# Kernel tuning notes

Measured on AMD Instinct MI355X. Metric: run time of the kernel, lower is better.

The kernel has to match this reference:

```python
import jax, jax.numpy as jnp
import numpy as np

N_NODES = 200000
N_EDGES = 12800000
C = 5  # channels
RADIUS = 0.05
CONSUME_RADIUS = RADIUS * 2
ACCEL_SCALE = 0.01
MAX_VEL = 0.1
CONSUME_EDGES_REQ = 3
EDGES_TO_STAY_ALIVE = 1
NEG_SLOPE = 0.2  # GATConv leaky_relu slope


def setup_inputs() -> dict:
    key = jax.random.key(0)
    ks = jax.random.split(key, 16)
    x = jax.random.normal(ks[0], (N_NODES, C), dtype=jnp.float32) * 0.1
    # column 4 is node type: 1 = cell, 0 = food
    is_cell = jax.random.bernoulli(ks[1], 0.9, (N_NODES,)).astype(jnp.float32)
    x = x.at[:, 4].set(is_cell)
    edge_index = jax.random.randint(ks[2], (2, N_EDGES), 0, N_NODES, dtype=jnp.int32)
    # edge_attr: [distance, is_cell_edge]
    dist = jax.random.uniform(ks[3], (N_EDGES,), dtype=jnp.float32) * 0.2
    cell_edge = jax.random.bernoulli(ks[4], 0.8, (N_EDGES,)).astype(jnp.float32)
    edge_attr = jnp.stack([dist, cell_edge], axis=1)
    s = 1.0 / np.sqrt(C)
    W = jax.random.normal(ks[5], (C, C), dtype=jnp.float32) * s        # GAT lin (shared src/dst)
    att_src = jax.random.normal(ks[6], (C,), dtype=jnp.float32) * s
    att_dst = jax.random.normal(ks[7], (C,), dtype=jnp.float32) * s
    We = jax.random.normal(ks[8], (2, C), dtype=jnp.float32) * 0.7      # lin_edge
    att_edge = jax.random.normal(ks[9], (C,), dtype=jnp.float32) * s
    gat_bias = jnp.zeros((C,), dtype=jnp.float32)
    W1 = jax.random.normal(ks[10], (C, C), dtype=jnp.float32) * s
    b1 = jnp.zeros((C,), dtype=jnp.float32)
    W2 = jax.random.normal(ks[11], (C, 2), dtype=jnp.float32) * s
    b2 = jnp.zeros((2,), dtype=jnp.float32)
    return {"x": x, "edge_index": edge_index, "edge_attr": edge_attr,
            "W": W, "att_src": att_src, "att_dst": att_dst, "We": We,
            "att_edge": att_edge, "gat_bias": gat_bias,
            "W1": W1, "b1": b1, "W2": W2, "b2": b2}


def _gat_conv(x, edge_index, edge_attr, W, att_src, att_dst, We, att_edge, gat_bias):
    # PyG GATConv, heads=1, edge_dim=2: softmax over incoming edges of each dst node
    n = x.shape[0]
    src, dst = edge_index[0], edge_index[1]
    hs = x @ W                                   # [N, C]
    a_src = hs @ att_src                         # [N]
    a_dst = hs @ att_dst                         # [N]
    a_e = (edge_attr @ We) @ att_edge            # [E]
    logits = jax.nn.leaky_relu(a_src[src] + a_dst[dst] + a_e, NEG_SLOPE)  # [E]
    m = jax.ops.segment_max(logits, dst, num_segments=n)                  # [N]
    ev = jnp.exp(logits - m[dst])
    denom = jax.ops.segment_sum(ev, dst, num_segments=n)                  # [N]
    alpha = ev / jnp.maximum(denom, 1e-16)[dst]
    out = jax.ops.segment_sum(hs[src] * alpha[:, None], dst, num_segments=n)
    return out + gat_bias


def reference(x, edge_index, edge_attr, W, att_src, att_dst, We, att_edge, gat_bias, W1, b1, W2, b2):
    n = x.shape[0]
    src = edge_index[0]
    # convolve: GAT -> MLP -> *2-1
    h = _gat_conv(x, edge_index, edge_attr, W, att_src, att_dst, We, att_edge, gat_bias)
    h = jax.nn.relu(jax.nn.relu(h @ W1 + b1) @ W2 + b2)
    h = h * 2.0 - 1.0                             # [N, 2]
    # only cells (type==1) accelerate
    food_mask = (x[:, 4] == 1).astype(jnp.float32)
    accel = h * ACCEL_SCALE * food_mask[:, None]
    velocity = jnp.clip(x[:, 2:4] + accel, -MAX_VEL, MAX_VEL)
    positions = x[:, :2] + velocity
    new_x = jnp.concatenate([positions, velocity, x[:, 4:]], axis=1)  # [N, 5]
    # border cost
    eps = 1e-6
    out_mask = (jnp.abs(positions) > 1).astype(jnp.float32)
    border_cost = jnp.sum(jnp.log(jnp.abs(positions) + eps) * out_mask)
    # consume-food mask: food nodes with >=3 close edges
    close = (edge_attr[:, 0] < CONSUME_RADIUS).astype(jnp.int32)
    close_cnt = jax.ops.segment_sum(close, src, num_segments=n)
    consumed = (x[:, 4] == 0) & (close_cnt >= CONSUME_EDGES_REQ)
    # island-cell mask: cells with < 1 cell-edge
    cell_e = (edge_attr[:, 1] == 1).astype(jnp.int32)
    cell_cnt = jax.ops.segment_sum(cell_e, src, num_segments=n)
    dead = (x[:, 4] == 1) & (cell_cnt < EDGES_TO_STAY_ALIVE)
    return (new_x, jnp.mean(jnp.abs(velocity), axis=0), border_cost,
            jnp.sum(consumed.astype(jnp.int32)), jnp.sum(dead.astype(jnp.int32)))
```

## Files before the change

kernel.cpp:

```cpp
#include <hip/hip_runtime.h>
#include <math.h>

#define NEG_SLOPE   0.2f
#define CONSUME_R   0.1f
#define ACCEL_SCALE 0.01f
#define MAX_VEL     0.1f

#define NBUCK  2048
#define TPB    512
#define EPT    16
#define EPB    (TPB*EPT)
#define MAXNPB 128
#define SMAX   6912

typedef float    v2f __attribute__((ext_vector_type(2)));
typedef unsigned v2u __attribute__((ext_vector_type(2)));

__device__ __forceinline__ unsigned bucket_of(unsigned v, unsigned npb, float inv_npb,
                                              unsigned* loc)
{
    unsigned b = (unsigned)((float)v * inv_npb);
    unsigned lo = b * npb;
    if (v < lo)            { --b; lo -= npb; }
    else if (v >= lo + npb){ ++b; lo += npb; }
    *loc = v - lo;
    return b;
}

__device__ __forceinline__ int slice_of(int blk, int NB)
{
    int q = NB >> 3, r = NB & 7;
    int xcd = blk & 7, idx = blk >> 3;
    return (xcd < r ? xcd * (q + 1) : r * (q + 1) + (xcd - r) * q) + idx;
}

__global__ __launch_bounds__(256) void k_pre(
    const float* __restrict__ x, const float* __restrict__ W,
    const float* __restrict__ att_src, const float* __restrict__ att_dst,
    uint4* __restrict__ npack, float* __restrict__ aD,
    float* __restrict__ scal, int n)
{
    int i = blockIdx.x * 256 + threadIdx.x;
    if (i >= n) return;
    if (i < 16) scal[i] = 0.f;
    float xr[5];
#pragma unroll
    for (int k = 0; k < 5; ++k) xr[k] = x[(size_t)i * 5 + k];
    float hs[5];
#pragma unroll
    for (int c = 0; c < 5; ++c) {
        float s = 0.f;
#pragma unroll
        for (int k = 0; k < 5; ++k) s += xr[k] * W[k * 5 + c];
        hs[c] = s;
    }
    float a_s = 0.f, a_d = 0.f;
#pragma unroll
    for (int c = 0; c < 5; ++c) { a_s += hs[c] * att_src[c]; a_d += hs[c] * att_dst[c]; }
    aD[i] = a_d;
    unsigned b[5];
#pragma unroll
    for (int c = 0; c < 5; ++c) {
        unsigned u = __float_as_uint(hs[c]);
        b[c] = (u + 0x7FFFu + ((u >> 16) & 1u)) >> 16;
    }
    npack[i] = make_uint4(b[0] | (b[1] << 16), b[2] | (b[3] << 16), b[4],
                          __float_as_uint(a_s));
}

__global__ __launch_bounds__(TPB) void k_hist(
    const int* __restrict__ dst, int* __restrict__ hist,
    int NB, int nE, unsigned npb, float inv_npb)
{
    __shared__ int hd[NBUCK];
    int t = threadIdx.x, blk = blockIdx.x;
    for (int j = t; j < NBUCK; j += TPB) hd[j] = 0;
    __syncthreads();
    int base = blk * EPB;
#pragma unroll 4
    for (int k = 0; k < EPT; ++k) {
        int e = base + k * TPB + t;
        if (e < nE) {
            unsigned loc;
            unsigned bd = bucket_of((unsigned)__builtin_nontemporal_load(dst + e),
                                    npb, inv_npb, &loc);
            atomicAdd(&hd[bd], 1);
        }
    }
    __syncthreads();
    for (int j = t; j < NBUCK; j += TPB) hist[(size_t)blk * NBUCK + j] = hd[j];
}

__global__ __launch_bounds__(256) void k_scanA(
    int* __restrict__ hist, int* __restrict__ rowtot, int NB)
{
    int b = (blockIdx.x & 7) * (NBUCK / 8) + (blockIdx.x >> 3);
    int t = threadIdx.x;
    __shared__ int ws4[4];
    __shared__ int carry;
    if (t == 0) carry = 0;
    __syncthreads();
    for (int base = 0; base < NB; base += 256) {
        int i = base + t;
        int v = (i < NB) ? hist[(size_t)i * NBUCK + b] : 0;
        int xv = v;
#pragma unroll
        for (int off = 1; off < 64; off <<= 1) {
            int y = __shfl_up(xv, off);
            if ((t & 63) >= off) xv += y;
        }
        if ((t & 63) == 63) ws4[t >> 6] = xv;
        __syncthreads();
        int add = 0;
        for (int w = 0; w < (t >> 6); ++w) add += ws4[w];
        int total = ws4[0] + ws4[1] + ws4[2] + ws4[3];
        if (i < NB) hist[(size_t)i * NBUCK + b] = carry + xv + add - v;
        __syncthreads();
        if (t == 0) carry += total;
        __syncthreads();
    }
    if (t == 0) rowtot[b] = carry;
}

__global__ __launch_bounds__(1024) void k_scanB(
    const int* __restrict__ rowtot, int* __restrict__ bbase)
{
    __shared__ int wsum[16], wex[16];
    int t = threadIdx.x;
    int a = rowtot[2 * t], b2 = rowtot[2 * t + 1];
    int v = a + b2;
    int xv = v;
#pragma unroll
    for (int off = 1; off < 64; off <<= 1) {
        int y = __shfl_up(xv, off);
        if ((t & 63) >= off) xv += y;
    }
    if ((t & 63) == 63) wsum[t >> 6] = xv;
    __syncthreads();
    if (t == 0) { int r = 0; for (int w = 0; w < 16; ++w) { wex[w] = r; r += wsum[w]; } }
    __syncthreads();
    int excl = xv - v + wex[t >> 6];
    bbase[2 * t] = excl;
    bbase[2 * t + 1] = excl + a;
    if (t == 1023) bbase[NBUCK] = excl + v;
}

__global__ __launch_bounds__(TPB) void k_scatter(
    const int* __restrict__ ei, const float* __restrict__ ea,
    const float* __restrict__ We, const float* __restrict__ att_edge,
    const int* __restrict__ hist, const int* __restrict__ bbase,
    unsigned* __restrict__ payD, unsigned short* __restrict__ payS,
    int* __restrict__ dirS, int NB, int nE, unsigned npb, float inv_npb)
{
    __shared__ int cD[NBUCK], cS[NBUCK], baseS[NBUCK], dirGl[NBUCK];
    __shared__ unsigned short paySL[EPB];
    __shared__ int wsc[8], wex[8];
    int t = threadIdx.x;
    int sl = slice_of(blockIdx.x, NB);
    for (int j = t; j < NBUCK; j += TPB) {
        cD[j] = 0; cS[j] = 0;
        dirGl[j] = bbase[j] + hist[(size_t)sl * NBUCK + j];
    }
    __syncthreads();

    float v0 = 0.f, v1 = 0.f;
#pragma unroll
    for (int c = 0; c < 5; ++c) { v0 += We[c] * att_edge[c]; v1 += We[5 + c] * att_edge[c]; }

    int base = sl * EPB;
    unsigned key[EPT], bb[EPT];
    float ae[EPT];

#pragma unroll
    for (int k = 0; k < EPT; ++k) {
        int e = base + k * TPB + t;
        bb[k] = 0;
        if (e < nE) {
            unsigned s = (unsigned)__builtin_nontemporal_load(ei + e);
            unsigned d = (unsigned)__builtin_nontemporal_load(ei + nE + e);
            v2f at = __builtin_nontemporal_load((const v2f*)ea + e);
            unsigned dloc, sloc;
            unsigned bd = bucket_of(d, npb, inv_npb, &dloc);
            unsigned bs = bucket_of(s, npb, inv_npb, &sloc);
            ae[k]  = at.x * v0 + at.y * v1;
            key[k] = s | (dloc << 18);
            bool close = at.x < CONSUME_R;
            bool cell  = (at.y == 1.0f);
            bb[k] = bd | (bs << 11) | (close ? (1u << 22) : 0u)
                       | (cell ? (1u << 23) : 0u) | (1u << 24);
            if (close || cell) atomicAdd(&cS[bs], 1);
        }
    }
    __syncthreads();

    {
        int a0 = cS[4 * t], a1 = cS[4 * t + 1], a2 = cS[4 * t + 2], a3 = cS[4 * t + 3];
        int lsum = a0 + a1 + a2 + a3;
        int xv = lsum;
#pragma unroll
        for (int off = 1; off < 64; off <<= 1) {
            int y = __shfl_up(xv, off);
            if ((t & 63) >= off) xv += y;
        }
        if ((t & 63) == 63) wsc[t >> 6] = xv;
        __syncthreads();
        if (t == 0) { int r = 0; for (int w = 0; w < 8; ++w) { wex[w] = r; r += wsc[w]; } }
        __syncthreads();
        int b0 = xv - lsum + wex[t >> 6];
        baseS[4 * t]     = b0;
        baseS[4 * t + 1] = b0 + a0;
        baseS[4 * t + 2] = b0 + a0 + a1;
        baseS[4 * t + 3] = b0 + a0 + a1 + a2;
    }
    __syncthreads();
    for (int j = t; j < NBUCK; j += TPB) {
        dirS[(size_t)j * NB + sl] = baseS[j] | (cS[j] << 16);
        cS[j] = 0;
    }
    __syncthreads();

#pragma unroll
    for (int k = 0; k < EPT; ++k) {
        if (bb[k] & (1u << 24)) {
            unsigned bd = bb[k] & 0x7FFu;
            int r = atomicAdd(&cD[bd], 1);
            v2u rec; rec.x = key[k]; rec.y = __float_as_uint(ae[k]);
            ((v2u*)payD)[dirGl[bd] + r] = rec;
            if (bb[k] & 0xC00000u) {
                unsigned bs = (bb[k] >> 11) & 0x7FFu;
                unsigned sloc = (key[k] & 0x3FFFFu) - bs * npb;
                unsigned srec = sloc | ((bb[k] >> 22) & 1u) << 11 | ((bb[k] >> 23) & 1u) << 12;
                int r2 = atomicAdd(&cS[bs], 1);
                paySL[baseS[bs] + r2] = (unsigned short)srec;
            }
        }
    }
    __syncthreads();

    unsigned* pgs = (unsigned*)(payS + (size_t)sl * EPB);
    const unsigned* pls = (const unsigned*)paySL;
#pragma unroll
    for (int j = 0; j < EPB / 2 / TPB; ++j) pgs[j * TPB + t] = pls[j * TPB + t];
}

__global__ __launch_bounds__(1024) void k_sortred(
    const unsigned* __restrict__ payD, const unsigned short* __restrict__ payS,
    const int* __restrict__ bbase, const int* __restrict__ dirS,
    const uint4* __restrict__ npack, const float* __restrict__ aD,
    const float* __restrict__ x,
    const float* __restrict__ gat_bias, const float* __restrict__ W1,
    const float* __restrict__ b1, const float* __restrict__ W2,
    const float* __restrict__ b2,
    float* __restrict__ out, float* __restrict__ scal,
    int NB, int n, int npb)
{
    __shared__ unsigned srt[SMAX * 2];
    __shared__ float accf[MAXNPB * 6];
    __shared__ float aDl[MAXNPB];
    __shared__ int cntL[MAXNPB], offL[MAXNPB], cnts[MAXNPB];
    __shared__ float sm[16][5];

    int b = blockIdx.x, t = threadIdx.x;
    int lo = bbase[b], hi = bbase[b + 1], span = hi - lo;
    int first = b * npb;
    int nodes = n - first; if (nodes > npb) nodes = npb; if (nodes < 0) nodes = 0;

    for (int j = t; j < npb; j += 1024) { cntL[j] = 0; cnts[j] = 0; }
    for (int j = t; j < npb * 6; j += 1024) accf[j] = 0.f;
    for (int j = t; j < nodes; j += 1024) aDl[j] = aD[first + j];
    __syncthreads();

    int grp = t >> 4, l16 = t & 15;

    if (span <= SMAX) {
        for (int idx = lo + t; idx < hi; idx += 1024) {
            unsigned w0 = payD[2 * (size_t)idx];
            atomicAdd(&cntL[(w0 >> 18) & 0x3FFu], 1);
        }
        __syncthreads();
        if (t == 0) {
            int r = 0;
            for (int j = 0; j < nodes; ++j) { offL[j] = r; r += cntL[j]; cntL[j] = 0; }
        }
        __syncthreads();
        for (int idx = lo + t; idx < hi; idx += 1024) {
            v2u rec = *((const v2u*)payD + idx);
            unsigned dl = (rec.x >> 18) & 0x3FFu;
            int r = atomicAdd(&cntL[dl], 1);
            int p = offL[dl] + r;
            srt[2 * p] = rec.x; srt[2 * p + 1] = rec.y;
        }
        __syncthreads();
        for (int nd = grp; nd < nodes; nd += 64) {
            int s = offL[nd], e = s + cntL[nd];
            float s0 = 0.f, s1 = 0.f, s2 = 0.f, s3 = 0.f, s4 = 0.f, s5 = 0.f;
            for (int j = s + l16; j < e; j += 16) {
                unsigned w0 = srt[2 * j];
                float aev = __uint_as_float(srt[2 * j + 1]);
                uint4 hp = npack[w0 & 0x3FFFFu];
                float z = __uint_as_float(hp.w) + aev + aDl[nd];
                float l = z > 0.f ? z : NEG_SLOPE * z;
                float ev = __expf(l);
                s0 += ev * __uint_as_float(hp.x << 16);
                s1 += ev * __uint_as_float(hp.x & 0xFFFF0000u);
                s2 += ev * __uint_as_float(hp.y << 16);
                s3 += ev * __uint_as_float(hp.y & 0xFFFF0000u);
                s4 += ev * __uint_as_float(hp.z << 16);
                s5 += ev;
            }
#pragma unroll
            for (int m = 1; m < 16; m <<= 1) {
                s0 += __shfl_xor(s0, m);
                s1 += __shfl_xor(s1, m);
                s2 += __shfl_xor(s2, m);
                s3 += __shfl_xor(s3, m);
                s4 += __shfl_xor(s4, m);
                s5 += __shfl_xor(s5, m);
            }
            if (l16 == 0) {
                float* a = &accf[nd * 6];
                a[0] += s0; a[1] += s1; a[2] += s2; a[3] += s3; a[4] += s4; a[5] += s5;
            }
        }
    } else {
        for (int idx = lo + t; idx < hi; idx += 1024) {
            v2u rec = *((const v2u*)payD + idx);
            unsigned dl = (rec.x >> 18) & 0x3FFu;
            uint4 hp = npack[rec.x & 0x3FFFFu];
            float z = __uint_as_float(hp.w) + __uint_as_float(rec.y) + aDl[dl];
            float l = z > 0.f ? z : NEG_SLOPE * z;
            float ev = __expf(l);
            float* a = &accf[dl * 6];
            atomicAdd(a + 0, ev * __uint_as_float(hp.x << 16));
            atomicAdd(a + 1, ev * __uint_as_float(hp.x & 0xFFFF0000u));
            atomicAdd(a + 2, ev * __uint_as_float(hp.y << 16));
            atomicAdd(a + 3, ev * __uint_as_float(hp.y & 0xFFFF0000u));
            atomicAdd(a + 4, ev * __uint_as_float(hp.z << 16));
            atomicAdd(a + 5, ev);
        }
    }

    for (int s = grp; s < NB; s += 64) {
        int pk = dirS[(size_t)b * NB + s];
        int st = pk & 0xFFFF, cn = ((unsigned)pk) >> 16;
        size_t sb = (size_t)s * EPB;
        for (int j = st + l16; j < st + cn; j += 16) {
            unsigned sr = payS[sb + j];
            int add = (int)((sr >> 11) & 1u) | (int)(((sr >> 12) & 1u) << 16);
            atomicAdd(&cnts[sr & 0x3FFu], add);
        }
    }
    __syncthreads();

    float part[5] = {0.f, 0.f, 0.f, 0.f, 0.f};
    if (t < nodes) {
        int i = first + t;
        const float* a = &accf[t * 6];
        float inv = 1.0f / fmaxf(a[5], 1e-16f);
        float h[5];
#pragma unroll
        for (int c = 0; c < 5; ++c) h[c] = a[c] * inv + gat_bias[c];
        float tt[5];
#pragma unroll
        for (int c = 0; c < 5; ++c) {
            float s = b1[c];
#pragma unroll
            for (int k = 0; k < 5; ++k) s += h[k] * W1[k * 5 + c];
            tt[c] = fmaxf(s, 0.f);
        }
        float u0 = b2[0], u1 = b2[1];
#pragma unroll
        for (int k = 0; k < 5; ++k) { u0 += tt[k] * W2[k * 2]; u1 += tt[k] * W2[k * 2 + 1]; }
        u0 = fmaxf(u0, 0.f) * 2.f - 1.f;
        u1 = fmaxf(u1, 0.f) * 2.f - 1.f;

        float px = x[(size_t)i * 5],     py = x[(size_t)i * 5 + 1];
        float vx = x[(size_t)i * 5 + 2], vy = x[(size_t)i * 5 + 3];
        float ty = x[(size_t)i * 5 + 4];
        float mask = (ty == 1.0f) ? 1.0f : 0.0f;
        float nvx = fminf(fmaxf(vx + u0 * ACCEL_SCALE * mask, -MAX_VEL), MAX_VEL);
        float nvy = fminf(fmaxf(vy + u1 * ACCEL_SCALE * mask, -MAX_VEL), MAX_VEL);
        float npx = px + nvx, npy = py + nvy;

        out[(size_t)i * 5]     = npx;
        out[(size_t)i * 5 + 1] = npy;
        out[(size_t)i * 5 + 2] = nvx;
        out[(size_t)i * 5 + 3] = nvy;
        out[(size_t)i * 5 + 4] = ty;

        part[0] = fabsf(nvx);
        part[1] = fabsf(nvy);
        float bc = 0.f;
        if (fabsf(npx) > 1.0f) bc += logf(fabsf(npx) + 1e-6f);
        if (fabsf(npy) > 1.0f) bc += logf(fabsf(npy) + 1e-6f);
        part[2] = bc;
        int c = cnts[t];
        part[3] = (ty == 0.0f && (c & 0xffff) >= 3) ? 1.f : 0.f;
        part[4] = (ty == 1.0f && (c >> 16) < 1) ? 1.f : 0.f;
    }

#pragma unroll
    for (int q = 0; q < 5; ++q)
#pragma unroll
        for (int off = 32; off > 0; off >>= 1)
            part[q] += __shfl_down(part[q], off);
    int lane = t & 63, wid = t >> 6;
    if (lane == 0)
#pragma unroll
        for (int q = 0; q < 5; ++q) sm[wid][q] = part[q];
    __syncthreads();
    if (t == 0) {
#pragma unroll
        for (int q = 0; q < 5; ++q) {
            float s = 0.f;
#pragma unroll
            for (int w = 0; w < 16; ++w) s += sm[w][q];
            unsafeAtomicAdd(scal + q, s);
        }
    }
}

__global__ void k_tail(const float* __restrict__ scal, float* __restrict__ out, int n)
{
    if (threadIdx.x == 0 && blockIdx.x == 0) {
        size_t base = (size_t)n * 5;
        float invn = 1.0f / (float)n;
        out[base + 0] = scal[0] * invn;
        out[base + 1] = scal[1] * invn;
        out[base + 2] = scal[2];
        out[base + 3] = scal[3];
        out[base + 4] = scal[4];
    }
}

__global__ __launch_bounds__(256) void k_node_pre_fb(
    const float* __restrict__ x, const float* __restrict__ W,
    const float* __restrict__ att_src, const float* __restrict__ att_dst,
    float* __restrict__ npack, int n)
{
    int i = blockIdx.x * 256 + threadIdx.x;
    if (i >= n) return;
    float xr[5];
#pragma unroll
    for (int k = 0; k < 5; ++k) xr[k] = x[(size_t)i * 5 + k];
    float hs[5];
#pragma unroll
    for (int c = 0; c < 5; ++c) {
        float s = 0.f;
#pragma unroll
        for (int k = 0; k < 5; ++k) s += xr[k] * W[k * 5 + c];
        hs[c] = s;
    }
    float a_s = 0.f, a_d = 0.f;
#pragma unroll
    for (int c = 0; c < 5; ++c) { a_s += hs[c] * att_src[c]; a_d += hs[c] * att_dst[c]; }
    *(float4*)(npack + (size_t)i * 8)     = make_float4(hs[0], hs[1], hs[2], hs[3]);
    *(float4*)(npack + (size_t)i * 8 + 4) = make_float4(hs[4], a_s, a_d, 0.f);
}

__global__ __launch_bounds__(256) void k_edge_fb(
    const int* __restrict__ ei, const float* __restrict__ ea,
    const float* __restrict__ We, const float* __restrict__ att_edge,
    const float* __restrict__ npack, float* __restrict__ acc,
    int* __restrict__ cnt, int nE)
{
    int e = blockIdx.x * 256 + threadIdx.x;
    if (e >= nE) return;
    float v0 = 0.f, v1 = 0.f;
#pragma unroll
    for (int c = 0; c < 5; ++c) { v0 += We[c] * att_edge[c]; v1 += We[5 + c] * att_edge[c]; }
    int s = ei[e];
    int d = ei[nE + e];
    float2 at = *(const float2*)(ea + (size_t)e * 2);
    const float4 p0 = *(const float4*)(npack + (size_t)s * 8);
    const float2 p1 = *(const float2*)(npack + (size_t)s * 8 + 4);
    float a_dst_d = npack[(size_t)d * 8 + 6];
    float z = p1.y + a_dst_d + (at.x * v0 + at.y * v1);
    float l = z > 0.f ? z : NEG_SLOPE * z;
    float ev = __expf(l);
    float* ad = acc + (size_t)d * 8;
    unsafeAtomicAdd(ad + 0, ev * p0.x);
    unsafeAtomicAdd(ad + 1, ev * p0.y);
    unsafeAtomicAdd(ad + 2, ev * p0.z);
    unsafeAtomicAdd(ad + 3, ev * p0.w);
    unsafeAtomicAdd(ad + 4, ev * p1.x);
    unsafeAtomicAdd(ad + 5, ev);
    int cb = (at.x < CONSUME_R ? 1 : 0) | (at.y == 1.0f ? (1 << 16) : 0);
    if (cb) atomicAdd(cnt + s, cb);
}

__global__ __launch_bounds__(256) void k_final_fb(
    const float* __restrict__ x, const float* __restrict__ acc,
    const int* __restrict__ cnt,
    const float* __restrict__ gat_bias, const float* __restrict__ W1,
    const float* __restrict__ b1, const float* __restrict__ W2,
    const float* __restrict__ b2,
    float* __restrict__ out, float* __restrict__ scal, int n)
{
    int i = blockIdx.x * 256 + threadIdx.x;
    float part[5] = {0.f, 0.f, 0.f, 0.f, 0.f};
    if (i < n) {
        const float* a = acc + (size_t)i * 8;
        float inv = 1.0f / fmaxf(a[5], 1e-16f);
        float h[5];
#pragma unroll
        for (int c = 0; c < 5; ++c) h[c] = a[c] * inv + gat_bias[c];
        float tt[5];
#pragma unroll
        for (int c = 0; c < 5; ++c) {
            float s = b1[c];
#pragma unroll
            for (int k = 0; k < 5; ++k) s += h[k] * W1[k * 5 + c];
            tt[c] = fmaxf(s, 0.f);
        }
        float u0 = b2[0], u1 = b2[1];
#pragma unroll
        for (int k = 0; k < 5; ++k) { u0 += tt[k] * W2[k * 2]; u1 += tt[k] * W2[k * 2 + 1]; }
        u0 = fmaxf(u0, 0.f) * 2.f - 1.f;
        u1 = fmaxf(u1, 0.f) * 2.f - 1.f;
        float px = x[(size_t)i * 5],     py = x[(size_t)i * 5 + 1];
        float vx = x[(size_t)i * 5 + 2], vy = x[(size_t)i * 5 + 3];
        float ty = x[(size_t)i * 5 + 4];
        float mask = (ty == 1.0f) ? 1.0f : 0.0f;
        float nvx = fminf(fmaxf(vx + u0 * ACCEL_SCALE * mask, -MAX_VEL), MAX_VEL);
        float nvy = fminf(fmaxf(vy + u1 * ACCEL_SCALE * mask, -MAX_VEL), MAX_VEL);
        float npx = px + nvx, npy = py + nvy;
        out[(size_t)i * 5]     = npx;
        out[(size_t)i * 5 + 1] = npy;
        out[(size_t)i * 5 + 2] = nvx;
        out[(size_t)i * 5 + 3] = nvy;
        out[(size_t)i * 5 + 4] = ty;
        part[0] = fabsf(nvx);
        part[1] = fabsf(nvy);
        float bc = 0.f;
        if (fabsf(npx) > 1.0f) bc += logf(fabsf(npx) + 1e-6f);
        if (fabsf(npy) > 1.0f) bc += logf(fabsf(npy) + 1e-6f);
        part[2] = bc;
        int c = cnt[i];
        part[3] = (ty == 0.0f && (c & 0xffff) >= 3) ? 1.f : 0.f;
        part[4] = (ty == 1.0f && (c >> 16) < 1) ? 1.f : 0.f;
    }
    __shared__ float sm[4][5];
#pragma unroll
    for (int q = 0; q < 5; ++q)
#pragma unroll
        for (int off = 32; off > 0; off >>= 1)
            part[q] += __shfl_down(part[q], off);
    int lane = threadIdx.x & 63, wid = threadIdx.x >> 6;
    if (lane == 0)
#pragma unroll
        for (int q = 0; q < 5; ++q) sm[wid][q] = part[q];
    __syncthreads();
    if (threadIdx.x == 0) {
#pragma unroll
        for (int q = 0; q < 5; ++q)
            unsafeAtomicAdd(scal + q, sm[0][q] + sm[1][q] + sm[2][q] + sm[3][q]);
    }
}

extern "C" void kernel_launch(void* const* d_in, const int* in_sizes, int n_in,
                              void* d_out, int out_size, void* d_ws, size_t ws_size,
                              hipStream_t stream)
{
    const float* x        = (const float*)d_in[0];
    const int*   ei       = (const int*)  d_in[1];
    const float* ea       = (const float*)d_in[2];
    const float* W        = (const float*)d_in[3];
    const float* att_src  = (const float*)d_in[4];
    const float* att_dst  = (const float*)d_in[5];
    const float* We       = (const float*)d_in[6];
    const float* att_edge = (const float*)d_in[7];
    const float* gat_bias = (const float*)d_in[8];
    const float* b1       = (const float*)d_in[10];
    const float* W1       = (const float*)d_in[9];
    const float* W2       = (const float*)d_in[11];
    const float* b2       = (const float*)d_in[12];

    int n  = in_sizes[0] / 5;
    int nE = in_sizes[1] / 2;

    int npb = (n + NBUCK - 1) / NBUCK;
    int NB = (nE + EPB - 1) / EPB;
    float inv_npb = 1.0f / (float)npb;

    size_t o = 0;
    auto alloc = [&](size_t bytes) { size_t r = o; o = (o + bytes + 63) & ~63ULL; return r; };
    size_t off_npack = alloc((size_t)n * 16);
    size_t off_aD    = alloc((size_t)n * 4);
    size_t off_hist  = alloc((size_t)NB * NBUCK * 4);
    size_t off_rtot  = alloc((size_t)NBUCK * 4);
    size_t off_bbase = alloc((size_t)(NBUCK + 1) * 4);
    size_t off_dirS  = alloc((size_t)NB * NBUCK * 4);
    size_t off_payS  = alloc((size_t)NB * EPB * 2);
    size_t off_scal  = alloc(64);
    size_t off_payD  = alloc((size_t)nE * 8);
    size_t need = o;

    char* wsb = (char*)d_ws;
    bool ok_shape = (n < (1 << 18)) && (npb <= MAXNPB) && (NB >= 1);
    bool fast = ok_shape && (ws_size >= need);

    if (fast) {
        uint4*          npack = (uint4*)(wsb + off_npack);
        float*          aD    = (float*)(wsb + off_aD);
        int*            hist  = (int*)(wsb + off_hist);
        int*            rtot  = (int*)(wsb + off_rtot);
        int*            bbase = (int*)(wsb + off_bbase);
        int*            dirS  = (int*)(wsb + off_dirS);
        unsigned short* payS  = (unsigned short*)(wsb + off_payS);
        float*          scal  = (float*)(wsb + off_scal);
        unsigned*       payD  = (unsigned*)(wsb + off_payD);

        k_pre<<<(n + 255) / 256, 256, 0, stream>>>(x, W, att_src, att_dst, npack, aD,
                                                   scal, n);
        k_hist<<<NB, TPB, 0, stream>>>(ei + nE, hist, NB, nE, (unsigned)npb, inv_npb);
        k_scanA<<<NBUCK, 256, 0, stream>>>(hist, rtot, NB);
        k_scanB<<<1, 1024, 0, stream>>>(rtot, bbase);
        k_scatter<<<NB, TPB, 0, stream>>>(ei, ea, We, att_edge, hist, bbase,
                                          payD, payS, dirS, NB, nE, (unsigned)npb, inv_npb);
        k_sortred<<<NBUCK, 1024, 0, stream>>>(payD, payS, bbase, dirS, npack, aD, x,
                                              gat_bias, W1, b1, W2, b2,
                                              (float*)d_out, scal, NB, n, npb);
        k_tail<<<1, 64, 0, stream>>>(scal, (float*)d_out, n);
    } else {
        float* ws    = (float*)d_ws;
        float* npk   = ws;
        float* acc   = ws + (size_t)n * 8;
        int*   cnt   = (int*)(acc + (size_t)n * 8);
        float* scal  = (float*)(cnt + n);
        size_t zbytes = ((size_t)n * 8 + (size_t)n + 8) * sizeof(float);
        hipMemsetAsync(acc, 0, zbytes, stream);
        k_node_pre_fb<<<(n + 255) / 256, 256, 0, stream>>>(x, W, att_src, att_dst, npk, n);
        k_edge_fb<<<(nE + 255) / 256, 256, 0, stream>>>(ei, ea, We, att_edge, npk,
                                                        acc, cnt, nE);
        k_final_fb<<<(n + 255) / 256, 256, 0, stream>>>(x, acc, cnt, gat_bias, W1, b1,
                                                        W2, b2, (float*)d_out, scal, n);
        k_tail<<<1, 64, 0, stream>>>(scal, (float*)d_out, n);
    }
}
```

Measured before the change: 603.1 us.

## Cache bucket records in registers, parallel-scan offsets, and interleave block-to-bucket mapping

```diff
diff --git a/kernel.cpp b/kernel.cpp
--- a/kernel.cpp
+++ b/kernel.cpp
@@ -260,7 +260,8 @@
     __shared__ int cntL[MAXNPB], offL[MAXNPB], cnts[MAXNPB];
     __shared__ float sm[16][5];
 
-    int b = blockIdx.x, t = threadIdx.x;
+    int b = (blockIdx.x & 7) * (NBUCK / 8) + (blockIdx.x >> 3);
+    int t = threadIdx.x;
     int lo = bbase[b], hi = bbase[b + 1], span = hi - lo;
     int first = b * npb;
     int nodes = n - first; if (nodes > npb) nodes = npb; if (nodes < 0) nodes = 0;
@@ -273,22 +274,41 @@
     int grp = t >> 4, l16 = t & 15;
 
     if (span <= SMAX) {
-        for (int idx = lo + t; idx < hi; idx += 1024) {
-            unsigned w0 = payD[2 * (size_t)idx];
-            atomicAdd(&cntL[(w0 >> 18) & 0x3FFu], 1);
-        }
-        __syncthreads();
-        if (t == 0) {
-            int r = 0;
-            for (int j = 0; j < nodes; ++j) { offL[j] = r; r += cntL[j]; cntL[j] = 0; }
-        }
-        __syncthreads();
-        for (int idx = lo + t; idx < hi; idx += 1024) {
-            v2u rec = *((const v2u*)payD + idx);
-            unsigned dl = (rec.x >> 18) & 0x3FFu;
-            int r = atomicAdd(&cntL[dl], 1);
-            int p = offL[dl] + r;
-            srt[2 * p] = rec.x; srt[2 * p + 1] = rec.y;
+        v2u recs[7];
+#pragma unroll
+        for (int k = 0; k < 7; ++k) {
+            int idx = lo + k * 1024 + t;
+            if (idx < hi) {
+                recs[k] = __builtin_nontemporal_load((const v2u*)payD + idx);
+                atomicAdd(&cntL[(recs[k].x >> 18) & 0x3FFu], 1);
+            }
+        }
+        __syncthreads();
+        if (t < 64) {
+            int i0 = 2 * t, i1 = 2 * t + 1;
+            int a0 = (i0 < npb) ? cntL[i0] : 0;
+            int a1 = (i1 < npb) ? cntL[i1] : 0;
+            int v = a0 + a1;
+            int xv = v;
+#pragma unroll
+            for (int off = 1; off < 64; off <<= 1) {
+                int y = __shfl_up(xv, off);
+                if (t >= off) xv += y;
+            }
+            int ex = xv - v;
+            if (i0 < npb) { offL[i0] = ex;      cntL[i0] = 0; }
+            if (i1 < npb) { offL[i1] = ex + a0; cntL[i1] = 0; }
+        }
+        __syncthreads();
+#pragma unroll
+        for (int k = 0; k < 7; ++k) {
+            int idx = lo + k * 1024 + t;
+            if (idx < hi) {
+                unsigned dl = (recs[k].x >> 18) & 0x3FFu;
+                int r = atomicAdd(&cntL[dl], 1);
+                int p = offL[dl] + r;
+                srt[2 * p] = recs[k].x; srt[2 * p + 1] = recs[k].y;
+            }
         }
         __syncthreads();
         for (int nd = grp; nd < nodes; nd += 64) {
```

Result: slower. 643.3 us (+6.7%).
